# Kernel optimization log

Hardware: AMD Instinct MI355X
Metric: run time of the kernel (lower is better)

The kernel has to match this reference:

```python
import jax, jax.numpy as jnp
import numpy as np

B, H, S, DK = 4, 16, 1024, 64


def setup_inputs() -> dict:
    key = jax.random.key(0)
    kq, kk, kv, km = jax.random.split(key, 4)
    q = jax.random.normal(kq, (B, H, S, DK), dtype=jnp.float32)
    k = jax.random.normal(kk, (B, H, S, DK), dtype=jnp.float32)
    v = jax.random.normal(kv, (B, H, S, DK), dtype=jnp.float32)
    mask = jax.random.randint(km, (B, 1, 1, S), 0, 2).astype(jnp.int32)
    return {"q": q, "k": k, "v": v, "mask": mask}


def reference(q, k, v, mask):
    dk = q.shape[-1]
    scale = 1.0 / np.sqrt(dk).astype(np.float32)
    # [B,H,S,S] scores
    qk = jnp.einsum("bhqd,bhkd->bhqk", q, k) * scale
    qk = jnp.where(mask == 0, jnp.float32(-10000.0), qk)
    attn_weight = jax.nn.softmax(qk, axis=-1)
    # NOTE: faithful to source bug — uses raw masked scores qk, not attn_weight
    output = jnp.einsum("bhqk,bhkd->bhqd", qk, v)
    return (output, attn_weight)
```

## Files before the change

kernel.cpp:

```cpp
#include <hip/hip_runtime.h>


typedef __attribute__((ext_vector_type(4))) float floatx4;
typedef __attribute__((ext_vector_type(8))) short shortx8;
typedef __attribute__((ext_vector_type(8))) unsigned short ushortx8;
typedef __attribute__((ext_vector_type(4))) int intx4;

#define S_ 1024
#define D_ 64
#define NELEM_ 4194304
#define ATTN_OFF 4194304
#define SCN 1040
#define QT 32

__device__ __forceinline__ unsigned short f32_to_bf16(float f) {
    union { float f; unsigned u; } a; a.f = f;
    unsigned u = a.u;
    u += 0x7fffu + ((u >> 16) & 1u);
    return (unsigned short)(u >> 16);
}

__device__ __forceinline__ float bf16_to_f32(unsigned short h) {
    union { unsigned u; float f; } a; a.u = ((unsigned)h) << 16;
    return a.f;
}

__device__ __forceinline__ ushortx8 pack8u(floatx4 a, floatx4 b) {
    ushortx8 r;
    r[0] = f32_to_bf16(a[0]); r[1] = f32_to_bf16(a[1]);
    r[2] = f32_to_bf16(a[2]); r[3] = f32_to_bf16(a[3]);
    r[4] = f32_to_bf16(b[0]); r[5] = f32_to_bf16(b[1]);
    r[6] = f32_to_bf16(b[2]); r[7] = f32_to_bf16(b[3]);
    return r;
}

__global__ __launch_bounds__(256) void pack_kv(const float* __restrict__ k,
                                               const float* __restrict__ v,
                                               unsigned short* __restrict__ kbt,
                                               unsigned short* __restrict__ vtp) {
    __shared__ float tile[64][65];
    if (blockIdx.x < 1024) {
        int g = blockIdx.x * 256 + threadIdx.x;
        int lane = g & 63;
        int kt   = (g >> 6) & 63;
        int bh   = g >> 12;
        int quad = lane >> 4;
        int l15  = lane & 15;
        const float* src = k + ((size_t)(bh * S_ + kt * 16 + l15)) * D_ + quad * 8;
        floatx4 f0 = *(const floatx4*)(src);
        floatx4 f1 = *(const floatx4*)(src + 4);
        floatx4 f2 = *(const floatx4*)(src + 32);
        floatx4 f3 = *(const floatx4*)(src + 36);
        unsigned short* dst = kbt + (size_t)g * 16;
        *(ushortx8*)(dst)     = pack8u(f0, f1);
        *(ushortx8*)(dst + 8) = pack8u(f2, f3);
    } else {
        int blk = blockIdx.x - 1024;
        int bh = blk >> 4;
        int s0 = (blk & 15) << 6;
        int tid = threadIdx.x;
        int r  = tid >> 2;
        int c0 = (tid & 3) << 4;
        const float* src = v + ((size_t)(bh * S_ + s0 + r)) * D_ + c0;
        #pragma unroll
        for (int j = 0; j < 4; ++j) {
            floatx4 f = *(const floatx4*)(src + j * 4);
            tile[r][c0 + j*4 + 0] = f[0];
            tile[r][c0 + j*4 + 1] = f[1];
            tile[r][c0 + j*4 + 2] = f[2];
            tile[r][c0 + j*4 + 3] = f[3];
        }
        __syncthreads();
        int d  = tid >> 2;
        int so = (tid & 3) << 4;
        int dt  = d >> 4;
        int l15 = d & 15;
        ushortx8 h0, h1;
        #pragma unroll
        for (int j = 0; j < 8; ++j) h0[j] = f32_to_bf16(tile[so + j][d]);
        #pragma unroll
        for (int j = 0; j < 8; ++j) h1[j] = f32_to_bf16(tile[so + 8 + j][d]);
        int sA = s0 + so;
        int ksA = sA >> 5, qA = (sA & 31) >> 3;
        int sB = sA + 8;
        int ksB = sB >> 5, qB = (sB & 31) >> 3;
        size_t baseA = ((((size_t)bh * 4 + dt) * 32 + ksA) * 64 + qA * 16 + l15) * 8;
        size_t baseB = ((((size_t)bh * 4 + dt) * 32 + ksB) * 64 + qB * 16 + l15) * 8;
        *(ushortx8*)(vtp + baseA) = h0;
        *(ushortx8*)(vtp + baseB) = h1;
    }
}

__global__ __launch_bounds__(512, 4) void attn_main(
    const float* __restrict__ q,
    const int* __restrict__ mask,
    const unsigned short* __restrict__ KbT,
    const unsigned short* __restrict__ VtP,
    float* __restrict__ out)
{
    __shared__ unsigned short sc[QT * SCN];
    __shared__ int msk[1024];

    int blk = blockIdx.x;
    int bh  = blk >> 5;
    int q0  = (blk & 31) << 5;
    int b   = bh >> 4;
    int tid = threadIdx.x;

    msk[tid]       = mask[(b << 10) + tid];
    msk[tid + 512] = mask[(b << 10) + tid + 512];

    int w    = tid >> 6;
    int lane = tid & 63;
    int l15  = lane & 15;
    int quad = lane >> 4;
    int rg   = w & 1;
    int cg   = w >> 1;

    shortx8 qf0, qf1;
    {
        const float* qb = q + ((size_t)(bh * S_ + q0 + rg * 16 + l15)) * D_ + quad * 8;
        floatx4 a0 = *(const floatx4*)(qb);
        floatx4 a1 = *(const floatx4*)(qb + 4);
        floatx4 b0 = *(const floatx4*)(qb + 32);
        floatx4 b1 = *(const floatx4*)(qb + 36);
        ushortx8 u0 = pack8u(a0, a1);
        ushortx8 u1 = pack8u(b0, b1);
        qf0 = (shortx8)u0;
        qf1 = (shortx8)u1;
    }

    __syncthreads();

    {
        const unsigned short* kb = KbT + ((size_t)bh * 64 * 64 + lane) * 16;
        #pragma unroll 4
        for (int t = 0; t < 16; ++t) {
            int kt = (cg << 4) + t;
            const unsigned short* p = kb + (size_t)kt * (64 * 16);
            shortx8 kf0 = *(const shortx8*)(p);
            shortx8 kf1 = *(const shortx8*)(p + 8);
            floatx4 acc = {0.f, 0.f, 0.f, 0.f};
            acc = __builtin_amdgcn_mfma_f32_16x16x32_bf16(qf0, kf0, acc, 0, 0, 0);
            acc = __builtin_amdgcn_mfma_f32_16x16x32_bf16(qf1, kf1, acc, 0, 0, 0);
            int n0 = kt << 4;
            int mv = msk[n0 + l15];
            int col = n0 + l15;
            #pragma unroll
            for (int r = 0; r < 4; ++r) {
                unsigned short h = mv ? f32_to_bf16(acc[r] * 0.125f)
                                      : (unsigned short)0xC61C;
                sc[(rg * 16 + quad * 4 + r) * SCN + col] = h;
            }
        }
    }
    __syncthreads();

    auto phase2 = [&]() {
        float* attnb = out + ATTN_OFF + ((size_t)(bh * S_ + q0)) * S_;
        for (int rr = 0; rr < 4; ++rr) {
            int row = (w << 2) + rr;
            const unsigned short* srow = sc + row * SCN;
            float vv[16];
            #pragma unroll
            for (int c = 0; c < 2; ++c) {
                ushortx8 h = *(const ushortx8*)(srow + (c << 9) + lane * 8);
                #pragma unroll
                for (int j = 0; j < 8; ++j) vv[c * 8 + j] = bf16_to_f32(h[j]);
            }
            float m = vv[0];
            #pragma unroll
            for (int j = 1; j < 16; ++j) m = fmaxf(m, vv[j]);
            #pragma unroll
            for (int off = 32; off; off >>= 1) m = fmaxf(m, __shfl_xor(m, off));
            float s = 0.f;
            #pragma unroll
            for (int j = 0; j < 16; ++j) { vv[j] = __expf(vv[j] - m); s += vv[j]; }
            #pragma unroll
            for (int off = 32; off; off >>= 1) s += __shfl_xor(s, off);
            float inv = 1.0f / s;
            float* arow = attnb + (size_t)row * S_ + lane * 8;
            #pragma unroll
            for (int c = 0; c < 2; ++c) {
                floatx4 o0 = { vv[c*8+0]*inv, vv[c*8+1]*inv, vv[c*8+2]*inv, vv[c*8+3]*inv };
                floatx4 o1 = { vv[c*8+4]*inv, vv[c*8+5]*inv, vv[c*8+6]*inv, vv[c*8+7]*inv };
                *(floatx4*)(arow + (c << 9))     = o0;
                *(floatx4*)(arow + (c << 9) + 4) = o1;
            }
        }
    };
    auto phase3 = [&]() {
        const unsigned short* vb = VtP + (((size_t)bh * 4 + cg) * 32) * (64 * 8) + lane * 8;
        const unsigned short* sr = sc + (rg * 16 + l15) * SCN + quad * 8;
        floatx4 oacc = {0.f, 0.f, 0.f, 0.f};
        #pragma unroll 4
        for (int ks = 0; ks < 32; ++ks) {
            shortx8 af = *(const shortx8*)(sr + (ks << 5));
            shortx8 bf = *(const shortx8*)(vb + (ks << 9));
            oacc = __builtin_amdgcn_mfma_f32_16x16x32_bf16(af, bf, oacc, 0, 0, 0);
        }
        float* ob = out + ((size_t)(bh * S_ + q0 + rg * 16 + (quad << 2))) * D_
                        + (cg << 4) + l15;
        #pragma unroll
        for (int r = 0; r < 4; ++r) ob[(size_t)r * D_] = oacc[r];
    };
    if (w & 1) { phase3(); phase2(); }
    else       { phase2(); phase3(); }
}

extern "C" void kernel_launch(void* const* d_in, const int* in_sizes, int n_in,
                              void* d_out, int out_size, void* d_ws, size_t ws_size,
                              hipStream_t stream) {
    const float* q   = (const float*)d_in[0];
    const float* k   = (const float*)d_in[1];
    const float* v   = (const float*)d_in[2];
    const int* mask  = (const int*)d_in[3];
    float* out = (float*)d_out;
    unsigned short* KbT = (unsigned short*)d_ws;
    unsigned short* VtP = KbT + NELEM_;
    pack_kv<<<2048, 256, 0, stream>>>(k, v, KbT, VtP);
    attn_main<<<2048, 512, 0, stream>>>(q, mask, KbT, VtP, out);
}
```

Measured before the change: 366.3 us.

## Remap blocks across XCDs, share K tiles over both row groups, nontemporal attn stores

Result: slower. 376.9 us (+2.9%).

```diff
diff --git a/kernel.cpp b/kernel.cpp
--- a/kernel.cpp
+++ b/kernel.cpp
@@ -101,7 +101,7 @@
     __shared__ unsigned short sc[QT * SCN];
     __shared__ int msk[1024];
 
-    int blk = blockIdx.x;
+    int blk = ((blockIdx.x & 7) << 8) | (blockIdx.x >> 3);
     int bh  = blk >> 5;
     int q0  = (blk & 31) << 5;
     int b   = bh >> 4;
@@ -117,40 +117,51 @@
     int rg   = w & 1;
     int cg   = w >> 1;
 
-    shortx8 qf0, qf1;
+    shortx8 qf0a, qf1a, qf0b, qf1b;
     {
-        const float* qb = q + ((size_t)(bh * S_ + q0 + rg * 16 + l15)) * D_ + quad * 8;
-        floatx4 a0 = *(const floatx4*)(qb);
-        floatx4 a1 = *(const floatx4*)(qb + 4);
-        floatx4 b0 = *(const floatx4*)(qb + 32);
-        floatx4 b1 = *(const floatx4*)(qb + 36);
-        ushortx8 u0 = pack8u(a0, a1);
-        ushortx8 u1 = pack8u(b0, b1);
-        qf0 = (shortx8)u0;
-        qf1 = (shortx8)u1;
+        const float* qb0 = q + ((size_t)(bh * S_ + q0 + l15)) * D_ + quad * 8;
+        const float* qb1 = qb0 + (size_t)16 * D_;
+        floatx4 a0 = *(const floatx4*)(qb0);
+        floatx4 a1 = *(const floatx4*)(qb0 + 4);
+        floatx4 a2 = *(const floatx4*)(qb0 + 32);
+        floatx4 a3 = *(const floatx4*)(qb0 + 36);
+        qf0a = (shortx8)pack8u(a0, a1);
+        qf1a = (shortx8)pack8u(a2, a3);
+        floatx4 b0 = *(const floatx4*)(qb1);
+        floatx4 b1 = *(const floatx4*)(qb1 + 4);
+        floatx4 b2 = *(const floatx4*)(qb1 + 32);
+        floatx4 b3 = *(const floatx4*)(qb1 + 36);
+        qf0b = (shortx8)pack8u(b0, b1);
+        qf1b = (shortx8)pack8u(b2, b3);
     }
 
     __syncthreads();
 
     {
         const unsigned short* kb = KbT + ((size_t)bh * 64 * 64 + lane) * 16;
-        #pragma unroll 4
-        for (int t = 0; t < 16; ++t) {
-            int kt = (cg << 4) + t;
+        #pragma unroll 2
+        for (int t = 0; t < 8; ++t) {
+            int kt = (w << 3) + t;
             const unsigned short* p = kb + (size_t)kt * (64 * 16);
             shortx8 kf0 = *(const shortx8*)(p);
             shortx8 kf1 = *(const shortx8*)(p + 8);
-            floatx4 acc = {0.f, 0.f, 0.f, 0.f};
-            acc = __builtin_amdgcn_mfma_f32_16x16x32_bf16(qf0, kf0, acc, 0, 0, 0);
-            acc = __builtin_amdgcn_mfma_f32_16x16x32_bf16(qf1, kf1, acc, 0, 0, 0);
+            floatx4 acc0 = {0.f, 0.f, 0.f, 0.f};
+            floatx4 acc1 = {0.f, 0.f, 0.f, 0.f};
+            acc0 = __builtin_amdgcn_mfma_f32_16x16x32_bf16(qf0a, kf0, acc0, 0, 0, 0);
+            acc0 = __builtin_amdgcn_mfma_f32_16x16x32_bf16(qf1a, kf1, acc0, 0, 0, 0);
+            acc1 = __builtin_amdgcn_mfma_f32_16x16x32_bf16(qf0b, kf0, acc1, 0, 0, 0);
+            acc1 = __builtin_amdgcn_mfma_f32_16x16x32_bf16(qf1b, kf1, acc1, 0, 0, 0);
             int n0 = kt << 4;
             int mv = msk[n0 + l15];
             int col = n0 + l15;
             #pragma unroll
             for (int r = 0; r < 4; ++r) {
-                unsigned short h = mv ? f32_to_bf16(acc[r] * 0.125f)
-                                      : (unsigned short)0xC61C;
-                sc[(rg * 16 + quad * 4 + r) * SCN + col] = h;
+                unsigned short h0 = mv ? f32_to_bf16(acc0[r] * 0.125f)
+                                       : (unsigned short)0xC61C;
+                unsigned short h1 = mv ? f32_to_bf16(acc1[r] * 0.125f)
+                                       : (unsigned short)0xC61C;
+                sc[(quad * 4 + r) * SCN + col]        = h0;
+                sc[(16 + quad * 4 + r) * SCN + col]   = h1;
             }
         }
     }
@@ -184,8 +195,8 @@
             for (int c = 0; c < 2; ++c) {
                 floatx4 o0 = { vv[c*8+0]*inv, vv[c*8+1]*inv, vv[c*8+2]*inv, vv[c*8+3]*inv };
                 floatx4 o1 = { vv[c*8+4]*inv, vv[c*8+5]*inv, vv[c*8+6]*inv, vv[c*8+7]*inv };
-                *(floatx4*)(arow + (c << 9))     = o0;
-                *(floatx4*)(arow + (c << 9) + 4) = o1;
+                __builtin_nontemporal_store(o0, (floatx4*)(arow + (c << 9)));
+                __builtin_nontemporal_store(o1, (floatx4*)(arow + (c << 9) + 4));
             }
         }
     };
```

## Halve query tile per block and split warps between softmax and PV

Applied to the files above, without the earlier changes.

Result: slower. 376.3 us (+2.7%).

```diff
diff --git a/kernel.cpp b/kernel.cpp
--- a/kernel.cpp
+++ b/kernel.cpp
@@ -4,14 +4,13 @@
 typedef __attribute__((ext_vector_type(4))) float floatx4;
 typedef __attribute__((ext_vector_type(8))) short shortx8;
 typedef __attribute__((ext_vector_type(8))) unsigned short ushortx8;
-typedef __attribute__((ext_vector_type(4))) int intx4;
 
 #define S_ 1024
 #define D_ 64
 #define NELEM_ 4194304
 #define ATTN_OFF 4194304
-#define SCN 1040
-#define QT 32
+#define SCN 1048
+#define QT 16
 
 __device__ __forceinline__ unsigned short f32_to_bf16(float f) {
     union { float f; unsigned u; } a; a.f = f;
@@ -91,7 +90,7 @@
     }
 }
 
-__global__ __launch_bounds__(512, 4) void attn_main(
+__global__ __launch_bounds__(512, 8) void attn_main(
     const float* __restrict__ q,
     const int* __restrict__ mask,
     const unsigned short* __restrict__ KbT,
@@ -99,44 +98,35 @@
     float* __restrict__ out)
 {
     __shared__ unsigned short sc[QT * SCN];
-    __shared__ int msk[1024];
-
-    int blk = blockIdx.x;
-    int bh  = blk >> 5;
-    int q0  = (blk & 31) << 5;
+
+    int blk = ((blockIdx.x & 7) << 9) | (blockIdx.x >> 3);
+    int bh  = blk >> 6;
+    int q0  = (blk & 63) << 4;
     int b   = bh >> 4;
     int tid = threadIdx.x;
-
-    msk[tid]       = mask[(b << 10) + tid];
-    msk[tid + 512] = mask[(b << 10) + tid + 512];
 
     int w    = tid >> 6;
     int lane = tid & 63;
     int l15  = lane & 15;
     int quad = lane >> 4;
-    int rg   = w & 1;
-    int cg   = w >> 1;
+    const int* mrow = mask + (b << 10);
 
     shortx8 qf0, qf1;
     {
-        const float* qb = q + ((size_t)(bh * S_ + q0 + rg * 16 + l15)) * D_ + quad * 8;
+        const float* qb = q + ((size_t)(bh * S_ + q0 + l15)) * D_ + quad * 8;
         floatx4 a0 = *(const floatx4*)(qb);
         floatx4 a1 = *(const floatx4*)(qb + 4);
-        floatx4 b0 = *(const floatx4*)(qb + 32);
-        floatx4 b1 = *(const floatx4*)(qb + 36);
-        ushortx8 u0 = pack8u(a0, a1);
-        ushortx8 u1 = pack8u(b0, b1);
-        qf0 = (shortx8)u0;
-        qf1 = (shortx8)u1;
-    }
-
-    __syncthreads();
+        floatx4 a2 = *(const floatx4*)(qb + 32);
+        floatx4 a3 = *(const floatx4*)(qb + 36);
+        qf0 = (shortx8)pack8u(a0, a1);
+        qf1 = (shortx8)pack8u(a2, a3);
+    }
 
     {
         const unsigned short* kb = KbT + ((size_t)bh * 64 * 64 + lane) * 16;
-        #pragma unroll 4
-        for (int t = 0; t < 16; ++t) {
-            int kt = (cg << 4) + t;
+        #pragma unroll 2
+        for (int t = 0; t < 8; ++t) {
+            int kt = (w << 3) + t;
             const unsigned short* p = kb + (size_t)kt * (64 * 16);
             shortx8 kf0 = *(const shortx8*)(p);
             shortx8 kf1 = *(const shortx8*)(p + 8);
@@ -144,20 +134,21 @@
             acc = __builtin_amdgcn_mfma_f32_16x16x32_bf16(qf0, kf0, acc, 0, 0, 0);
             acc = __builtin_amdgcn_mfma_f32_16x16x32_bf16(qf1, kf1, acc, 0, 0, 0);
             int n0 = kt << 4;
-            int mv = msk[n0 + l15];
             int col = n0 + l15;
+            int mv = mrow[col];
             #pragma unroll
             for (int r = 0; r < 4; ++r) {
                 unsigned short h = mv ? f32_to_bf16(acc[r] * 0.125f)
                                       : (unsigned short)0xC61C;
-                sc[(rg * 16 + quad * 4 + r) * SCN + col] = h;
+                sc[(quad * 4 + r) * SCN + col] = h;
             }
         }
     }
     __syncthreads();
 
-    auto phase2 = [&]() {
+    if (w < 4) {
         float* attnb = out + ATTN_OFF + ((size_t)(bh * S_ + q0)) * S_;
+        #pragma unroll
         for (int rr = 0; rr < 4; ++rr) {
             int row = (w << 2) + rr;
             const unsigned short* srow = sc + row * SCN;
@@ -188,24 +179,22 @@
                 *(floatx4*)(arow + (c << 9) + 4) = o1;
             }
         }
-    };
-    auto phase3 = [&]() {
+    } else {
+        int cg = w - 4;
         const unsigned short* vb = VtP + (((size_t)bh * 4 + cg) * 32) * (64 * 8) + lane * 8;
-        const unsigned short* sr = sc + (rg * 16 + l15) * SCN + quad * 8;
+        const unsigned short* sr = sc + l15 * SCN + quad * 8;
         floatx4 oacc = {0.f, 0.f, 0.f, 0.f};
-        #pragma unroll 4
+        #pragma unroll 2
         for (int ks = 0; ks < 32; ++ks) {
             shortx8 af = *(const shortx8*)(sr + (ks << 5));
             shortx8 bf = *(const shortx8*)(vb + (ks << 9));
             oacc = __builtin_amdgcn_mfma_f32_16x16x32_bf16(af, bf, oacc, 0, 0, 0);
         }
-        float* ob = out + ((size_t)(bh * S_ + q0 + rg * 16 + (quad << 2))) * D_
+        float* ob = out + ((size_t)(bh * S_ + q0 + (quad << 2))) * D_
                         + (cg << 4) + l15;
         #pragma unroll
         for (int r = 0; r < 4; ++r) ob[(size_t)r * D_] = oacc[r];
-    };
-    if (w & 1) { phase3(); phase2(); }
-    else       { phase2(); phase3(); }
+    }
 }
 
 extern "C" void kernel_launch(void* const* d_in, const int* in_sizes, int n_in,
@@ -219,5 +208,5 @@
     unsigned short* KbT = (unsigned short*)d_ws;
     unsigned short* VtP = KbT + NELEM_;
     pack_kv<<<2048, 256, 0, stream>>>(k, v, KbT, VtP);
-    attn_main<<<2048, 512, 0, stream>>>(q, mask, KbT, VtP, out);
-}
+    attn_main<<<4096, 512, 0, stream>>>(q, mask, KbT, VtP, out);
+}
```
